# Performance work log

Measured on AMD Instinct MI355X. Metric: run time of the kernel, lower is better.

## Reference

```python
import jax, jax.numpy as jnp
import numpy as np

EPS = 1e-3  # keras BatchNormalization default epsilon


def _conv1x1(x, W, b):
    # x: (b, h, w, cin), W: (cin, cout)
    return jnp.einsum('bhwc,cd->bhwd', x, W) + b


def _bn(x, gamma, beta, mean, var):
    # inference-mode batch norm (moving statistics)
    return gamma * (x - mean) * jax.lax.rsqrt(var + EPS) + beta


def setup_inputs() -> dict:
    key = jax.random.key(0)
    ks = jax.random.split(key, 20)
    C, Ci = 512, 256
    B, Ha, Wa, Hd, Wd = 8, 32, 32, 64, 64
    s_in = 1.0 / np.sqrt(C)
    s_ic = 1.0 / np.sqrt(Ci)
    inp = {
        'detect': jax.random.normal(ks[0], (B, Hd, Wd, C), jnp.float32),
        'aim': jax.random.normal(ks[1], (B, Ha, Wa, C), jnp.float32),
        # g, theta, phi: C -> Ci 1x1 convs
        'Wg': jax.random.normal(ks[2], (C, Ci), jnp.float32) * s_in,
        'bg': jnp.zeros((Ci,), jnp.float32),
        'Wt': jax.random.normal(ks[3], (C, Ci), jnp.float32) * s_in,
        'bt': jnp.zeros((Ci,), jnp.float32),
        'Wp': jax.random.normal(ks[4], (C, Ci), jnp.float32) * s_in,
        'bp': jnp.zeros((Ci,), jnp.float32),
        # W branch: Ci -> C conv + BN
        'Ww': jax.random.normal(ks[5], (Ci, C), jnp.float32) * s_ic,
        'bw': jnp.zeros((C,), jnp.float32),
        'gw': jnp.ones((C,), jnp.float32),
        'betw': jnp.zeros((C,), jnp.float32),
        'mw': jax.random.normal(ks[6], (C,), jnp.float32) * 0.1,
        'vw': jax.random.uniform(ks[7], (C,), jnp.float32, 0.5, 1.5),
        # Q branch: Ci -> C conv + BN
        'Wq': jax.random.normal(ks[8], (Ci, C), jnp.float32) * s_ic,
        'bq': jnp.zeros((C,), jnp.float32),
        'gq': jnp.ones((C,), jnp.float32),
        'betq': jnp.zeros((C,), jnp.float32),
        'mq': jax.random.normal(ks[9], (C,), jnp.float32) * 0.1,
        'vq': jax.random.uniform(ks[10], (C,), jnp.float32, 0.5, 1.5),
    }
    return inp


def reference(detect, aim, Wg, bg, Wt, bt, Wp, bp,
              Ww, bw, gw, betw, mw, vw,
              Wq, bq, gq, betq, mq, vq):
    B, Ha, Wa, C = aim.shape
    _, Hd, Wd, _ = detect.shape
    Ci = Wg.shape[1]
    Na, Nd = Ha * Wa, Hd * Wd

    d_x = _conv1x1(detect, Wg, bg).reshape(B, Nd, Ci)     # (b, Nd, Ci)
    a_x = _conv1x1(aim, Wg, bg).reshape(B, Na, Ci)        # (b, Na, Ci)
    theta_x = _conv1x1(aim, Wt, bt).reshape(B, Na, Ci)    # (b, Na, Ci)
    phi_x = _conv1x1(detect, Wp, bp).reshape(B, Nd, Ci)   # (b, Nd, Ci)

    # affinity: (b, Na, Nd)
    f = jnp.einsum('bnc,bmc->bnm', theta_x, phi_x)
    f_div_C = f / Nd          # normalize by last dim of f
    fi_div_C = jnp.swapaxes(f, 1, 2) / Na  # (b, Nd, Na), normalized by its last dim

    non_aim = jnp.einsum('bnm,bmc->bnc', f_div_C, d_x).reshape(B, Ha, Wa, Ci)
    non_aim = _bn(_conv1x1(non_aim, Ww, bw), gw, betw, mw, vw) + aim

    non_det = jnp.einsum('bmn,bnc->bmc', fi_div_C, a_x).reshape(B, Hd, Wd, Ci)
    non_det = _bn(_conv1x1(non_det, Wq, bq), gq, betq, mq, vq) + detect

    return non_aim, non_det
```

## Files before the change

### kernel.cpp

```cpp
#include <hip/hip_runtime.h>

typedef unsigned short ushort_t;
typedef unsigned int uint32;
typedef __bf16 bf16x8 __attribute__((ext_vector_type(8)));
typedef float f32x4 __attribute__((ext_vector_type(4)));
typedef uint32 u32x4 __attribute__((ext_vector_type(4)));
typedef uint32 u32x2 __attribute__((ext_vector_type(2)));

typedef __attribute__((address_space(3))) uint32 as3_u32;
typedef const __attribute__((address_space(1))) uint32 as1_u32c;

__device__ __forceinline__ void gl_lds16(const ushort_t* g, ushort_t* l) {
    __builtin_amdgcn_global_load_lds((as1_u32c*)g, (as3_u32*)l, 16, 0, 0);
}

__device__ __forceinline__ float bf2f(ushort_t u) {
    uint32 x = ((uint32)u) << 16;
    return __builtin_bit_cast(float, x);
}
__device__ __forceinline__ ushort_t f2bf(float f) {
    uint32 x = __builtin_bit_cast(uint32, f);
    x += 0x7fffu + ((x >> 16) & 1u);
    return (ushort_t)(x >> 16);
}
__device__ __forceinline__ void ld4bf(const ushort_t* p, float* f) {
    const u32x2 w = *(const u32x2*)p;
    f[0] = bf2f((ushort_t)(w[0] & 0xffffu)); f[1] = bf2f((ushort_t)(w[0] >> 16));
    f[2] = bf2f((ushort_t)(w[1] & 0xffffu)); f[3] = bf2f((ushort_t)(w[1] >> 16));
}
__device__ __forceinline__ u32x2 pk4bf(const float* v) {
    u32x2 pk;
    pk[0] = (uint32)f2bf(v[0]) | ((uint32)f2bf(v[1]) << 16);
    pk[1] = (uint32)f2bf(v[2]) | ((uint32)f2bf(v[3]) << 16);
    return pk;
}

struct VecArgs { const void* s[14]; ushort_t* d[14]; int n[14]; };
__global__ void sniff_vec_kernel(const uint32* __restrict__ src, int* __restrict__ flag,
                                 VecArgs a) {
    __shared__ int cnt;
    if (threadIdx.x == 0) cnt = 0;
    __syncthreads();
    if (threadIdx.x < 64) {
        int weird = 0;
        for (int c = 0; c < 4; c++) {
            uint32 w = src[threadIdx.x * 4 + c];
            uint32 e = (w >> 7) & 0xFFu;
            weird += (e < 64u) || (e >= 192u);
        }
        if (weird) atomicAdd(&cnt, weird);
    }
    __syncthreads();
    const bool isf32 = (cnt > 32);
    if (threadIdx.x == 0) *flag = isf32 ? 1 : 0;
    const int t = threadIdx.x;
    for (int seg = 0; seg < 14; seg++) {
        const int n = a.n[seg];
        if (isf32) {
            const float* s = (const float*)a.s[seg];
            for (int i = t; i < n; i += 256) a.d[seg][i] = f2bf(s[i]);
        } else {
            const ushort_t* s = (const ushort_t*)a.s[seg];
            for (int i = t; i < n; i += 256) a.d[seg][i] = s[i];
        }
    }
}

struct WtArgs { const void* s[6]; ushort_t* d[6]; int R[6]; int C[6]; };
__global__ void canon_all(const void* __restrict__ dsrc, ushort_t* __restrict__ ddst,
                          const void* __restrict__ asrc, ushort_t* __restrict__ adst,
                          WtArgs wa, const int* __restrict__ flag) {
    const bool isf32 = (*flag != 0);
    const int b = blockIdx.x;
    if (b < 3072) {
        const void* src; ushort_t* dst; long n; int b0, nb;
        if (b < 2048) { src = dsrc; dst = ddst; n = 16777216; b0 = b; nb = 2048; }
        else          { src = asrc; dst = adst; n = 4194304;  b0 = b - 2048; nb = 1024; }
        long i = ((long)b0 * 256 + threadIdx.x) * 8;
        const long stride = (long)nb * 256 * 8;
        if (isf32) {
            const float* s = (const float*)src;
            for (; i < n; i += stride) {
                const f32x4 a = *(const f32x4*)(s + i);
                const f32x4 c = *(const f32x4*)(s + i + 4);
                u32x4 o;
                o[0] = (uint32)f2bf(a[0]) | ((uint32)f2bf(a[1]) << 16);
                o[1] = (uint32)f2bf(a[2]) | ((uint32)f2bf(a[3]) << 16);
                o[2] = (uint32)f2bf(c[0]) | ((uint32)f2bf(c[1]) << 16);
                o[3] = (uint32)f2bf(c[2]) | ((uint32)f2bf(c[3]) << 16);
                *(u32x4*)(dst + i) = o;
            }
        } else {
            const ushort_t* s = (const ushort_t*)src;
            for (; i < n; i += stride)
                *(u32x4*)(dst + i) = *(const u32x4*)(s + i);
        }
    } else {
        const int local = b - 3072;
        const int wsel = local >> 8;
        const int rem = local & 255;
        const int tr = rem >> 4, tc = rem & 15;
        const int R = wa.R[wsel], C = wa.C[wsel];
        if (tc * 32 >= C || tr * 32 >= R) return;
        __shared__ float s[32][33];
        const int t = threadIdx.x;
        const int r = t >> 3, c4 = (t & 7) * 4;
        const long sbase = (long)(tr * 32 + r) * C + tc * 32 + c4;
        if (isf32) {
            const float* S = (const float*)wa.s[wsel];
            const f32x4 v = *(const f32x4*)(S + sbase);
            for (int u = 0; u < 4; u++) s[r][c4 + u] = v[u];
        } else {
            const ushort_t* S = (const ushort_t*)wa.s[wsel];
            for (int u = 0; u < 4; u++) s[r][c4 + u] = bf2f(S[sbase + u]);
        }
        __syncthreads();
        float tv[4];
        for (int u = 0; u < 4; u++) tv[u] = s[c4 + u][r];
        *(u32x2*)(wa.d[wsel] + (long)(tc * 32 + r) * R + tr * 32 + c4) = pk4bf(tv);
    }
}

__global__ void reduce_t2_kernel(const float* __restrict__ P1, const float* __restrict__ P2,
                                 ushort_t* __restrict__ G1T, ushort_t* __restrict__ G2T) {
    __shared__ float s[32][33];
    const int zz = blockIdx.z;
    const float* P = (zz < 8) ? P1 : P2;
    ushort_t* out  = (zz < 8) ? G1T : G2T;
    const int b = zz & 7;
    const int tm = blockIdx.y, tn = blockIdx.x;
    const int t = threadIdx.x;
    const int r = t >> 3, c4 = (t & 7) * 4;
    const float* base = P + (long)b * 8 * 65536 + (long)(tm * 32 + r) * 256 + tn * 32 + c4;
    f32x4 acc = {0.f, 0.f, 0.f, 0.f};
    for (int kc = 0; kc < 8; kc++) acc += *(const f32x4*)(base + (long)kc * 65536);
    for (int u = 0; u < 4; u++) s[r][c4 + u] = acc[u];
    __syncthreads();
    float tv[4];
    for (int u = 0; u < 4; u++) tv[u] = s[c4 + u][r];
    *(u32x2*)(out + (long)b * 65536 + (long)(tn * 32 + r) * 256 + tm * 32 + c4) = pk4bf(tv);
}

#define BM 128
#define BN 128
#define BK 32
#define BIGN (1 << 30)

enum { EPI_BIAS = 0, EPI_BIASR = 1, EPI_SCALE = 2, EPI_BN = 3, EPI_PART = 4 };

struct GP {
    const ushort_t* A; const ushort_t* B; void* Cv; ushort_t* CT;
    const ushort_t* bias; const ushort_t* gamma; const ushort_t* beta;
    const ushort_t* mean; const ushort_t* var; const ushort_t* res;
    long coff, sA, sB, sC;
    int K, lda, ldb, ldc, cnmax, ldT;
    float alpha;
};
struct GP2 { GP g[2]; };

template <int EPI, bool DYNOUT, bool DUALT, bool SWAP>
__global__ __launch_bounds__(256) void gemm_nt(GP2 ga, int ysplit, int zsplit,
                                               const int* __restrict__ flag)
{
    __shared__ __align__(16) ushort_t As[BM * BK];
    __shared__ __align__(16) ushort_t Bs[BN * BK];

    const bool isf32 = DYNOUT ? (*flag != 0) : false;

    const uint32 gx = gridDim.x, gy = gridDim.y;
    const uint32 nwg = gx * gy * gridDim.z;
    const uint32 lid = blockIdx.x + gx * (blockIdx.y + gy * blockIdx.z);
    const uint32 swz = (lid & 7u) * (nwg >> 3) + (lid >> 3);
    const uint32 bx = swz % gx, t1 = swz / gx;
    int by = (int)(t1 % gy), bz = (int)(t1 / gy);

    int sel = 0;
    if (by >= ysplit) { by -= ysplit; sel = 1; }
    if (bz >= zsplit) { bz -= zsplit; sel = 1; }
    const GP& p = ga.g[sel];

    const ushort_t* A = p.A + (long)bz * p.sA;
    const ushort_t* B = p.B + (long)bz * p.sB;
    const long cbase = p.coff + (long)bz * p.sC;
    const int lda = p.lda, ldb = p.ldb, ldc = p.ldc, K = p.K;

    const int tid  = threadIdx.x;
    const int lane = tid & 63;
    const int w    = tid >> 6;
    const int wr   = w >> 1, wc = w & 1;
    const int lr   = lane & 15, q = lane >> 4;

    const int m0 = by * BM;
    const int n0 = bx * BN;

    const int lrow = lane >> 2, lu = lane & 3;
    const int us = (lu ^ ((lrow >> 1) & 3)) * 8;
    const int ra0 = w * 32 + lrow, ra1 = w * 32 + 16 + lrow;
    const ushort_t* Ar0 = A + (long)(m0 + ra0) * lda + us;
    const ushort_t* Ar1 = A + (long)(m0 + ra1) * lda + us;
    const ushort_t* Br0 = B + (long)(n0 + ra0) * ldb + us;
    const ushort_t* Br1 = B + (long)(n0 + ra1) * ldb + us;
    ushort_t* sA0 = &As[(w * 2 + 0) * 512];
    ushort_t* sA1 = &As[(w * 2 + 1) * 512];
    ushort_t* sB0 = &Bs[(w * 2 + 0) * 512];
    ushort_t* sB1 = &Bs[(w * 2 + 1) * 512];

    const int swq = (q ^ ((lr >> 1) & 3)) * 8;

    f32x4 acc[4][4];
#pragma unroll
    for (int i = 0; i < 4; i++)
#pragma unroll
        for (int j = 0; j < 4; j++) acc[i][j] = (f32x4){0.f, 0.f, 0.f, 0.f};

    for (int k0 = 0; k0 < K; k0 += BK) {
        gl_lds16(Ar0 + k0, sA0);
        gl_lds16(Ar1 + k0, sA1);
        gl_lds16(Br0 + k0, sB0);
        gl_lds16(Br1 + k0, sB1);
        __syncthreads();

        bf16x8 af[4], bfr[4];
#pragma unroll
        for (int i = 0; i < 4; i++)
            af[i] = __builtin_bit_cast(bf16x8,
                *(const u32x4*)(&As[(wr * 64 + i * 16 + lr) * BK + swq]));
#pragma unroll
        for (int j = 0; j < 4; j++)
            bfr[j] = __builtin_bit_cast(bf16x8,
                *(const u32x4*)(&Bs[(wc * 64 + j * 16 + lr) * BK + swq]));
#pragma unroll
        for (int i = 0; i < 4; i++)
#pragma unroll
            for (int j = 0; j < 4; j++) {
                if constexpr (SWAP)
                    acc[i][j] = __builtin_amdgcn_mfma_f32_16x16x32_bf16(bfr[j], af[i], acc[i][j], 0, 0, 0);
                else
                    acc[i][j] = __builtin_amdgcn_mfma_f32_16x16x32_bf16(af[i], bfr[j], acc[i][j], 0, 0, 0);
            }
        __syncthreads();
    }

    if constexpr (SWAP) {
#pragma unroll
        for (int j = 0; j < 4; j++) {
            const int coln = n0 + wc * 64 + j * 16 + q * 4;
            float sc4[4], sh4[4];
            if constexpr (EPI == EPI_BIAS) {
                float bb[4]; ld4bf(p.bias + coln, bb);
#pragma unroll
                for (int r = 0; r < 4; r++) { sc4[r] = 1.f; sh4[r] = bb[r]; }
            } else if constexpr (EPI == EPI_SCALE) {
#pragma unroll
                for (int r = 0; r < 4; r++) { sc4[r] = p.alpha; sh4[r] = 0.f; }
            } else if constexpr (EPI == EPI_BN) {
                float bb[4], g[4], bt[4], mn[4], vr[4];
                ld4bf(p.bias + coln, bb); ld4bf(p.gamma + coln, g); ld4bf(p.beta + coln, bt);
                ld4bf(p.mean + coln, mn); ld4bf(p.var + coln, vr);
#pragma unroll
                for (int r = 0; r < 4; r++) {
                    const float s = g[r] * rsqrtf(vr[r] + 1e-3f);
                    sc4[r] = s;
                    sh4[r] = s * bb[r] + bt[r] - s * mn[r];
                }
            }
#pragma unroll
            for (int i = 0; i < 4; i++) {
                const int row = m0 + wr * 64 + i * 16 + lr;
                const long off = cbase + (long)row * ldc + coln;
                float v[4];
#pragma unroll
                for (int r = 0; r < 4; r++) v[r] = acc[i][j][r];
                if constexpr (EPI == EPI_BIASR) {
                    const float bs = bf2f(p.bias[row]);
#pragma unroll
                    for (int r = 0; r < 4; r++) v[r] += bs;
                } else if constexpr (EPI == EPI_BN) {
                    float rs[4]; ld4bf(p.res + (long)row * ldc + coln, rs);
#pragma unroll
                    for (int r = 0; r < 4; r++) v[r] = sc4[r] * v[r] + sh4[r] + rs[r];
                } else if constexpr (EPI != EPI_PART) {
#pragma unroll
                    for (int r = 0; r < 4; r++) v[r] = sc4[r] * v[r] + sh4[r];
                }
                if constexpr (EPI == EPI_PART) {
                    *(f32x4*)((float*)p.Cv + off) = (f32x4){v[0], v[1], v[2], v[3]};
                } else if constexpr (DYNOUT) {
                    if (isf32) *(f32x4*)((float*)p.Cv + off) = (f32x4){v[0], v[1], v[2], v[3]};
                    else       *(u32x2*)((ushort_t*)p.Cv + off) = pk4bf(v);
                } else {
                    *(u32x2*)((ushort_t*)p.Cv + off) = pk4bf(v);
                }
            }
        }
    } else {
        const bool doC = (n0 < p.cnmax);
#pragma unroll
        for (int j = 0; j < 4; j++) {
            const int col = n0 + wc * 64 + j * 16 + lr;
            float bs = 0.f, sc = 1.f, sh = 0.f;
            if constexpr (EPI == EPI_BIAS || EPI == EPI_BN) bs = bf2f(p.bias[col]);
            if constexpr (EPI == EPI_BN) {
                const float g  = bf2f(p.gamma[col]);
                const float bt = bf2f(p.beta[col]);
                const float mn = bf2f(p.mean[col]);
                const float vr = bf2f(p.var[col]);
                sc = g * rsqrtf(vr + 1e-3f);
                sh = bt - sc * mn;
            }
#pragma unroll
            for (int i = 0; i < 4; i++) {
                const int rowbase = m0 + wr * 64 + i * 16 + q * 4;
                ushort_t tmp[4];
#pragma unroll
                for (int r = 0; r < 4; r++) {
                    const int row = rowbase + r;
                    float v = acc[i][j][r];
                    if constexpr (EPI == EPI_BIAS) v += bs;
                    else if constexpr (EPI == EPI_BIASR) v += bf2f(p.bias[row]);
                    else if constexpr (EPI == EPI_SCALE) v *= p.alpha;
                    else if constexpr (EPI == EPI_BN)
                        v = sc * (v + bs) + sh + bf2f(p.res[(long)row * ldc + col]);
                    const long off = cbase + (long)row * ldc + col;
                    if constexpr (EPI == EPI_PART) {
                        ((float*)p.Cv)[off] = v;
                    } else if constexpr (DYNOUT) {
                        if (isf32) ((float*)p.Cv)[off] = v;
                        else       ((ushort_t*)p.Cv)[off] = f2bf(v);
                    } else {
                        const ushort_t us2 = f2bf(v);
                        tmp[r] = us2;
                        if (doC) ((ushort_t*)p.Cv)[off] = us2;
                    }
                }
                if constexpr (DUALT) {
                    u32x2 pk;
                    pk[0] = (uint32)tmp[0] | ((uint32)tmp[1] << 16);
                    pk[1] = (uint32)tmp[2] | ((uint32)tmp[3] << 16);
                    *(u32x2*)(p.CT + (long)col * p.ldT + rowbase) = pk;
                }
            }
        }
    }
}

extern "C" void kernel_launch(void* const* d_in, const int* in_sizes, int n_in,
                              void* d_out, int out_size, void* d_ws, size_t ws_size,
                              hipStream_t stream)
{
    int* flag = (int*)d_ws;
    ushort_t* base = (ushort_t*)((char*)d_ws + 16);
    long o = 0;
    ushort_t* detect_c = base + o; o += 16777216;
    ushort_t* aim_c    = base + o; o += 4194304;
    ushort_t* WpgT = base + o; o += 262144;
    ushort_t* WtgT = base + o; o += 262144;
    ushort_t* WwT  = base + o; o += 131072;
    ushort_t* WqT  = base + o; o += 131072;
    ushort_t* bpg_c  = base + o; o += 512;
    ushort_t* btg_c  = base + o; o += 512;
    ushort_t* bw_c   = base + o; o += 512;
    ushort_t* gw_c   = base + o; o += 512;
    ushort_t* betw_c = base + o; o += 512;
    ushort_t* mw_c   = base + o; o += 512;
    ushort_t* vw_c   = base + o; o += 512;
    ushort_t* bq_c   = base + o; o += 512;
    ushort_t* gq_c   = base + o; o += 512;
    ushort_t* betq_c = base + o; o += 512;
    ushort_t* mq_c   = base + o; o += 512;
    ushort_t* vq_c   = base + o; o += 512;
    ushort_t* phi    = base + o; o += 8388608;
    ushort_t* PT     = base + o; o += 16777216;
    ushort_t* theta  = base + o; o += 2097152;
    ushort_t* TT     = base + o; o += 4194304;
    ushort_t* G1T    = base + o; o += 524288;
    ushort_t* G2T    = base + o; o += 524288;
    ushort_t* U      = base + o; o += 16777216;
    float* P1 = (float*)U;
    float* P2 = P1 + 4194304;
    ushort_t* na = U;
    ushort_t* nd = na + 2097152;
    ushort_t* phiT = PT;
    ushort_t* d_xT = PT + 8388608;
    ushort_t* thetaT = TT;
    ushort_t* a_xT = TT + 2097152;

    VecArgs va;
    const int vidx[14] = {7, 3, 5, 3, 9, 10, 11, 12, 13, 15, 16, 17, 18, 19};
    ushort_t* vdst[14] = {bpg_c, bpg_c + 256, btg_c, btg_c + 256,
                          bw_c, gw_c, betw_c, mw_c, vw_c,
                          bq_c, gq_c, betq_c, mq_c, vq_c};
    const int vn[14] = {256, 256, 256, 256, 512, 512, 512, 512, 512, 512, 512, 512, 512, 512};
    for (int i = 0; i < 14; i++) { va.s[i] = d_in[vidx[i]]; va.d[i] = vdst[i]; va.n[i] = vn[i]; }
    sniff_vec_kernel<<<1, 256, 0, stream>>>((const uint32*)d_in[0], flag, va);

    WtArgs wa;
    wa.s[0] = d_in[6];  wa.d[0] = WpgT;              wa.R[0] = 512; wa.C[0] = 256;
    wa.s[1] = d_in[2];  wa.d[1] = WpgT + 256 * 512;  wa.R[1] = 512; wa.C[1] = 256;
    wa.s[2] = d_in[4];  wa.d[2] = WtgT;              wa.R[2] = 512; wa.C[2] = 256;
    wa.s[3] = d_in[2];  wa.d[3] = WtgT + 256 * 512;  wa.R[3] = 512; wa.C[3] = 256;
    wa.s[4] = d_in[8];  wa.d[4] = WwT;               wa.R[4] = 256; wa.C[4] = 512;
    wa.s[5] = d_in[14]; wa.d[5] = WqT;               wa.R[5] = 256; wa.C[5] = 512;
    canon_all<<<4608, 256, 0, stream>>>(d_in[0], detect_c, d_in[1], aim_c, wa, flag);

    const dim3 blk(256);
    const ushort_t* np = nullptr;
    ushort_t* npm = nullptr;

    {
        GP2 g;
        g.g[0] = GP{detect_c, WpgT, phi, PT, bpg_c, np, np, np, np, np,
                    0, 0, 0, 0, 512, 512, 512, 256, 256, 32768, 1.f};
        g.g[1] = GP{aim_c, WtgT, theta, TT, btg_c, np, np, np, np, np,
                    0, 0, 0, 0, 512, 512, 512, 256, 256, 8192, 1.f};
        gemm_nt<EPI_BIAS, false, true, false><<<dim3(4, 320, 1), blk, 0, stream>>>(
            g, 256, BIGN, flag);
    }

    {
        GP2 g;
        g.g[0] = GP{phiT, d_xT, P1, npm, np, np, np, np, np, np,
                    0, 512, 512, 65536, 512, 32768, 32768, 256, BIGN, 0, 1.f};
        g.g[1] = GP{thetaT, a_xT, P2, npm, np, np, np, np, np, np,
                    0, 128, 128, 65536, 128, 8192, 8192, 256, BIGN, 0, 1.f};
        gemm_nt<EPI_PART, false, false, true><<<dim3(2, 2, 128), blk, 0, stream>>>(
            g, BIGN, 64, flag);
    }

    reduce_t2_kernel<<<dim3(8, 8, 16), blk, 0, stream>>>(P1, P2, G1T, G2T);

    {
        GP2 g;
        g.g[0] = GP{phi, G2T, nd, npm, np, np, np, np, np, np,
                    0, 1048576, 65536, 1048576, 256, 256, 256, 256, BIGN, 0, 1.f / 1024.f};
        g.g[1] = GP{theta, G1T, na, npm, np, np, np, np, np, np,
                    0, 262144, 65536, 262144, 256, 256, 256, 256, BIGN, 0, 1.f / 4096.f};
        gemm_nt<EPI_SCALE, false, false, true><<<dim3(2, 40, 8), blk, 0, stream>>>(
            g, 32, BIGN, flag);
    }

    {
        GP2 g;
        g.g[0] = GP{nd, WqT, d_out, npm, bq_c, gq_c, betq_c, mq_c, vq_c, detect_c,
                    8192L * 512, 0, 0, 0, 256, 256, 256, 512, BIGN, 0, 1.f};
        g.g[1] = GP{na, WwT, d_out, npm, bw_c, gw_c, betw_c, mw_c, vw_c, aim_c,
                    0, 0, 0, 0, 256, 256, 256, 512, BIGN, 0, 1.f};
        gemm_nt<EPI_BN, true, false, true><<<dim3(4, 320, 1), blk, 0, stream>>>(
            g, 256, BIGN, flag);
    }
}
```

Baseline: 368.5 us.

## Triple-buffer LDS tiles in gemm_nt with async prefetch two stages ahead

Replaces the single-buffered K loop, which loaded one tile, synchronised, computed and synchronised again, with a three-stage LDS ring. Tiles for step t+2 are fetched with global_load_lds while the MFMAs for step t run. Explicit vmcnt waits and a single barrier per iteration replace the two __syncthreads, hiding global-load latency behind compute. In exchange LDS use triples to 48KB per block, which can lower occupancy.

```diff
diff --git a/kernel.cpp b/kernel.cpp
--- a/kernel.cpp
+++ b/kernel.cpp
@@ -144,6 +144,8 @@
 #define BM 128
 #define BN 128
 #define BK 32
+#define LDSH (BM * BK)
+#define NBUF 3
 #define BIGN (1 << 30)
 
 enum { EPI_BIAS = 0, EPI_BIASR = 1, EPI_SCALE = 2, EPI_BN = 3, EPI_PART = 4 };
@@ -162,8 +164,8 @@
 __global__ __launch_bounds__(256) void gemm_nt(GP2 ga, int ysplit, int zsplit,
                                                const int* __restrict__ flag)
 {
-    __shared__ __align__(16) ushort_t As[BM * BK];
-    __shared__ __align__(16) ushort_t Bs[BN * BK];
+    __shared__ __align__(16) ushort_t As[NBUF * LDSH];
+    __shared__ __align__(16) ushort_t Bs[NBUF * LDSH];
 
     const bool isf32 = DYNOUT ? (*flag != 0) : false;
 
@@ -213,22 +215,43 @@
 #pragma unroll
         for (int j = 0; j < 4; j++) acc[i][j] = (f32x4){0.f, 0.f, 0.f, 0.f};
 
-    for (int k0 = 0; k0 < K; k0 += BK) {
-        gl_lds16(Ar0 + k0, sA0);
-        gl_lds16(Ar1 + k0, sA1);
-        gl_lds16(Br0 + k0, sB0);
-        gl_lds16(Br1 + k0, sB1);
-        __syncthreads();
-
+    const int nt = K / BK;
+
+    {
+        gl_lds16(Ar0, sA0); gl_lds16(Ar1, sA1);
+        gl_lds16(Br0, sB0); gl_lds16(Br1, sB1);
+        if (nt > 1) {
+            gl_lds16(Ar0 + BK, sA0 + LDSH); gl_lds16(Ar1 + BK, sA1 + LDSH);
+            gl_lds16(Br0 + BK, sB0 + LDSH); gl_lds16(Br1 + BK, sB1 + LDSH);
+        }
+    }
+
+    int c0 = 0, c2 = 2;
+    for (int t = 0; t < nt; ++t) {
+        if (t + 1 < nt) asm volatile("s_waitcnt vmcnt(4)" ::: "memory");
+        else            asm volatile("s_waitcnt vmcnt(0)" ::: "memory");
+        __builtin_amdgcn_s_barrier();
+        __builtin_amdgcn_sched_barrier(0);
+
+        if (t + 2 < nt) {
+            const int nb = c2 * LDSH;
+            const int kn = (t + 2) * BK;
+            gl_lds16(Ar0 + kn, sA0 + nb); gl_lds16(Ar1 + kn, sA1 + nb);
+            gl_lds16(Br0 + kn, sB0 + nb); gl_lds16(Br1 + kn, sB1 + nb);
+        }
+        __builtin_amdgcn_sched_barrier(0);
+
+        const ushort_t* Ab = As + c0 * LDSH;
+        const ushort_t* Bb = Bs + c0 * LDSH;
         bf16x8 af[4], bfr[4];
 #pragma unroll
         for (int i = 0; i < 4; i++)
             af[i] = __builtin_bit_cast(bf16x8,
-                *(const u32x4*)(&As[(wr * 64 + i * 16 + lr) * BK + swq]));
+                *(const u32x4*)(&Ab[(wr * 64 + i * 16 + lr) * BK + swq]));
 #pragma unroll
         for (int j = 0; j < 4; j++)
             bfr[j] = __builtin_bit_cast(bf16x8,
-                *(const u32x4*)(&Bs[(wc * 64 + j * 16 + lr) * BK + swq]));
+                *(const u32x4*)(&Bb[(wc * 64 + j * 16 + lr) * BK + swq]));
 #pragma unroll
         for (int i = 0; i < 4; i++)
 #pragma unroll
@@ -238,7 +261,10 @@
                 else
                     acc[i][j] = __builtin_amdgcn_mfma_f32_16x16x32_bf16(af[i], bfr[j], acc[i][j], 0, 0, 0);
             }
-        __syncthreads();
+        __builtin_amdgcn_sched_barrier(0);
+
+        c0 = (c0 + 1 == NBUF) ? 0 : c0 + 1;
+        c2 = (c2 + 1 == NBUF) ? 0 : c2 + 1;
     }
 
     if constexpr (SWAP) {
```

After: 361.9 us. About the same (-1.8%).

## Fuse all stages into one persistent kernel with grid-wide barriers

Applied to the files above, without the earlier changes.

Replaces the six separate launches (sniff, canonicalize, conv GEMM, partial GEMM, reduce, attention GEMM, output GEMM) with a single persistent kernel of 1280 workgroups. Stages are separated by atomic-counter grid barriers, and the dtype sniff is computed per block with wave shuffles. The goal is to remove launch gaps and per-kernel tail effects. In exchange it relies on all 1280 workgroups being co-resident (launch bounds 256,5) and pays spin-wait barrier costs, while some stages leave many blocks idle.

```diff
diff --git a/kernel.cpp b/kernel.cpp
--- a/kernel.cpp
+++ b/kernel.cpp
@@ -10,6 +10,8 @@
 typedef __attribute__((address_space(3))) uint32 as3_u32;
 typedef const __attribute__((address_space(1))) uint32 as1_u32c;
 
+#define NWG 1280
+
 __device__ __forceinline__ void gl_lds16(const ushort_t* g, ushort_t* l) {
     __builtin_amdgcn_global_load_lds((as1_u32c*)g, (as3_u32*)l, 16, 0, 0);
 }
@@ -35,115 +37,10 @@
     return pk;
 }
 
-struct VecArgs { const void* s[14]; ushort_t* d[14]; int n[14]; };
-__global__ void sniff_vec_kernel(const uint32* __restrict__ src, int* __restrict__ flag,
-                                 VecArgs a) {
-    __shared__ int cnt;
-    if (threadIdx.x == 0) cnt = 0;
-    __syncthreads();
-    if (threadIdx.x < 64) {
-        int weird = 0;
-        for (int c = 0; c < 4; c++) {
-            uint32 w = src[threadIdx.x * 4 + c];
-            uint32 e = (w >> 7) & 0xFFu;
-            weird += (e < 64u) || (e >= 192u);
-        }
-        if (weird) atomicAdd(&cnt, weird);
-    }
-    __syncthreads();
-    const bool isf32 = (cnt > 32);
-    if (threadIdx.x == 0) *flag = isf32 ? 1 : 0;
-    const int t = threadIdx.x;
-    for (int seg = 0; seg < 14; seg++) {
-        const int n = a.n[seg];
-        if (isf32) {
-            const float* s = (const float*)a.s[seg];
-            for (int i = t; i < n; i += 256) a.d[seg][i] = f2bf(s[i]);
-        } else {
-            const ushort_t* s = (const ushort_t*)a.s[seg];
-            for (int i = t; i < n; i += 256) a.d[seg][i] = s[i];
-        }
-    }
-}
-
-struct WtArgs { const void* s[6]; ushort_t* d[6]; int R[6]; int C[6]; };
-__global__ void canon_all(const void* __restrict__ dsrc, ushort_t* __restrict__ ddst,
-                          const void* __restrict__ asrc, ushort_t* __restrict__ adst,
-                          WtArgs wa, const int* __restrict__ flag) {
-    const bool isf32 = (*flag != 0);
-    const int b = blockIdx.x;
-    if (b < 3072) {
-        const void* src; ushort_t* dst; long n; int b0, nb;
-        if (b < 2048) { src = dsrc; dst = ddst; n = 16777216; b0 = b; nb = 2048; }
-        else          { src = asrc; dst = adst; n = 4194304;  b0 = b - 2048; nb = 1024; }
-        long i = ((long)b0 * 256 + threadIdx.x) * 8;
-        const long stride = (long)nb * 256 * 8;
-        if (isf32) {
-            const float* s = (const float*)src;
-            for (; i < n; i += stride) {
-                const f32x4 a = *(const f32x4*)(s + i);
-                const f32x4 c = *(const f32x4*)(s + i + 4);
-                u32x4 o;
-                o[0] = (uint32)f2bf(a[0]) | ((uint32)f2bf(a[1]) << 16);
-                o[1] = (uint32)f2bf(a[2]) | ((uint32)f2bf(a[3]) << 16);
-                o[2] = (uint32)f2bf(c[0]) | ((uint32)f2bf(c[1]) << 16);
-                o[3] = (uint32)f2bf(c[2]) | ((uint32)f2bf(c[3]) << 16);
-                *(u32x4*)(dst + i) = o;
-            }
-        } else {
-            const ushort_t* s = (const ushort_t*)src;
-            for (; i < n; i += stride)
-                *(u32x4*)(dst + i) = *(const u32x4*)(s + i);
-        }
-    } else {
-        const int local = b - 3072;
-        const int wsel = local >> 8;
-        const int rem = local & 255;
-        const int tr = rem >> 4, tc = rem & 15;
-        const int R = wa.R[wsel], C = wa.C[wsel];
-        if (tc * 32 >= C || tr * 32 >= R) return;
-        __shared__ float s[32][33];
-        const int t = threadIdx.x;
-        const int r = t >> 3, c4 = (t & 7) * 4;
-        const long sbase = (long)(tr * 32 + r) * C + tc * 32 + c4;
-        if (isf32) {
-            const float* S = (const float*)wa.s[wsel];
-            const f32x4 v = *(const f32x4*)(S + sbase);
-            for (int u = 0; u < 4; u++) s[r][c4 + u] = v[u];
-        } else {
-            const ushort_t* S = (const ushort_t*)wa.s[wsel];
-            for (int u = 0; u < 4; u++) s[r][c4 + u] = bf2f(S[sbase + u]);
-        }
-        __syncthreads();
-        float tv[4];
-        for (int u = 0; u < 4; u++) tv[u] = s[c4 + u][r];
-        *(u32x2*)(wa.d[wsel] + (long)(tc * 32 + r) * R + tr * 32 + c4) = pk4bf(tv);
-    }
-}
-
-__global__ void reduce_t2_kernel(const float* __restrict__ P1, const float* __restrict__ P2,
-                                 ushort_t* __restrict__ G1T, ushort_t* __restrict__ G2T) {
-    __shared__ float s[32][33];
-    const int zz = blockIdx.z;
-    const float* P = (zz < 8) ? P1 : P2;
-    ushort_t* out  = (zz < 8) ? G1T : G2T;
-    const int b = zz & 7;
-    const int tm = blockIdx.y, tn = blockIdx.x;
-    const int t = threadIdx.x;
-    const int r = t >> 3, c4 = (t & 7) * 4;
-    const float* base = P + (long)b * 8 * 65536 + (long)(tm * 32 + r) * 256 + tn * 32 + c4;
-    f32x4 acc = {0.f, 0.f, 0.f, 0.f};
-    for (int kc = 0; kc < 8; kc++) acc += *(const f32x4*)(base + (long)kc * 65536);
-    for (int u = 0; u < 4; u++) s[r][c4 + u] = acc[u];
-    __syncthreads();
-    float tv[4];
-    for (int u = 0; u < 4; u++) tv[u] = s[c4 + u][r];
-    *(u32x2*)(out + (long)b * 65536 + (long)(tn * 32 + r) * 256 + tm * 32 + c4) = pk4bf(tv);
-}
-
 #define BM 128
 #define BN 128
 #define BK 32
+#define LDSH (BM * BK)
 #define BIGN (1 << 30)
 
 enum { EPI_BIAS = 0, EPI_BIASR = 1, EPI_SCALE = 2, EPI_BN = 3, EPI_PART = 4 };
@@ -157,28 +54,138 @@
     float alpha;
 };
 struct GP2 { GP g[2]; };
+struct VecArgs { const void* s[14]; ushort_t* d[14]; int n[14]; };
+struct WtArgs { const void* s[6]; ushort_t* d[6]; int R[6]; int C[6]; };
+
+struct MegaArgs {
+    const void* in0; const void* in1;
+    ushort_t* det; ushort_t* aim;
+    VecArgs va; WtArgs wa;
+    GP2 conv, part, ndna, outs;
+    const float* P1; const float* P2; ushort_t* G1T; ushort_t* G2T;
+    uint32* bar;
+};
+
+__device__ __forceinline__ bool sniff(const void* in0) {
+    const uint32* s = (const uint32*)in0;
+    const int lane = threadIdx.x & 63;
+    int wd = 0;
+    for (int c = 0; c < 4; c++) {
+        const uint32 w = s[lane * 4 + c];
+        const uint32 e = (w >> 7) & 0xFFu;
+        wd += (e < 64u) || (e >= 192u);
+    }
+    for (int off = 32; off; off >>= 1) wd += __shfl_down(wd, off);
+    return __shfl(wd, 0) > 32;
+}
+
+__device__ void gbar(uint32* ctr) {
+    __syncthreads();
+    if (threadIdx.x == 0) {
+        __threadfence();
+        atomicAdd(ctr, 1u);
+        while (__hip_atomic_load(ctr, __ATOMIC_RELAXED, __HIP_MEMORY_SCOPE_AGENT) < NWG)
+            __builtin_amdgcn_s_sleep(4);
+        __threadfence();
+    }
+    __syncthreads();
+}
+
+__device__ __forceinline__ void decode(int bid, int nwg, int gx, int gy,
+                                       int ys, int zs,
+                                       int& bx, int& by, int& bz, int& sel) {
+    const uint32 swz = (uint32)(bid & 7) * (uint32)(nwg >> 3) + (uint32)(bid >> 3);
+    bx = (int)(swz % (uint32)gx);
+    const uint32 t1 = swz / (uint32)gx;
+    by = (int)(t1 % (uint32)gy);
+    bz = (int)(t1 / (uint32)gy);
+    sel = 0;
+    if (by >= ys) { by -= ys; sel = 1; }
+    if (bz >= zs) { bz -= zs; sel = 1; }
+}
+
+__device__ void canon_vb(const MegaArgs& a, int b, bool isf32, float (*st)[33]) {
+    if (b < 3072) {
+        const void* src; ushort_t* dst; long n; int b0, nb;
+        if (b < 2048) { src = a.in0; dst = a.det; n = 16777216; b0 = b; nb = 2048; }
+        else          { src = a.in1; dst = a.aim; n = 4194304;  b0 = b - 2048; nb = 1024; }
+        long i = ((long)b0 * 256 + threadIdx.x) * 8;
+        const long stride = (long)nb * 256 * 8;
+        if (isf32) {
+            const float* s = (const float*)src;
+            for (; i < n; i += stride) {
+                const f32x4 x = *(const f32x4*)(s + i);
+                const f32x4 y = *(const f32x4*)(s + i + 4);
+                u32x4 o;
+                o[0] = (uint32)f2bf(x[0]) | ((uint32)f2bf(x[1]) << 16);
+                o[1] = (uint32)f2bf(x[2]) | ((uint32)f2bf(x[3]) << 16);
+                o[2] = (uint32)f2bf(y[0]) | ((uint32)f2bf(y[1]) << 16);
+                o[3] = (uint32)f2bf(y[2]) | ((uint32)f2bf(y[3]) << 16);
+                *(u32x4*)(dst + i) = o;
+            }
+        } else {
+            const ushort_t* s = (const ushort_t*)src;
+            for (; i < n; i += stride)
+                *(u32x4*)(dst + i) = *(const u32x4*)(s + i);
+        }
+    } else if (b < 4608) {
+        const int local = b - 3072;
+        const int wsel = local >> 8;
+        const int rem = local & 255;
+        const int tr = rem >> 4, tc = rem & 15;
+        const int R = a.wa.R[wsel], C = a.wa.C[wsel];
+        if (tc * 32 < C && tr * 32 < R) {
+            const int t = threadIdx.x;
+            const int r = t >> 3, c4 = (t & 7) * 4;
+            const long sbase = (long)(tr * 32 + r) * C + tc * 32 + c4;
+            if (isf32) {
+                const float* S = (const float*)a.wa.s[wsel];
+                const f32x4 v = *(const f32x4*)(S + sbase);
+                for (int u = 0; u < 4; u++) st[r][c4 + u] = v[u];
+            } else {
+                const ushort_t* S = (const ushort_t*)a.wa.s[wsel];
+                for (int u = 0; u < 4; u++) st[r][c4 + u] = bf2f(S[sbase + u]);
+            }
+            __syncthreads();
+            float tv[4];
+            for (int u = 0; u < 4; u++) tv[u] = st[c4 + u][r];
+            *(u32x2*)(a.wa.d[wsel] + (long)(tc * 32 + r) * R + tr * 32 + c4) = pk4bf(tv);
+        }
+    } else {
+        const int t = threadIdx.x;
+        for (int seg = 0; seg < 14; seg++) {
+            const int n = a.va.n[seg];
+            if (isf32) {
+                const float* s = (const float*)a.va.s[seg];
+                for (int i = t; i < n; i += 256) a.va.d[seg][i] = f2bf(s[i]);
+            } else {
+                const ushort_t* s = (const ushort_t*)a.va.s[seg];
+                for (int i = t; i < n; i += 256) a.va.d[seg][i] = s[i];
+            }
+        }
+    }
+}
+
+__device__ void reduce_tile(const MegaArgs& a, int bid, float (*st)[33]) {
+    const int tn = bid & 7, tm = (bid >> 3) & 7, zz = bid >> 6;
+    const float* P = (zz < 8) ? a.P1 : a.P2;
+    ushort_t* out  = (zz < 8) ? a.G1T : a.G2T;
+    const int b = zz & 7;
+    const int t = threadIdx.x;
+    const int r = t >> 3, c4 = (t & 7) * 4;
+    const float* base = P + (long)b * 8 * 65536 + (long)(tm * 32 + r) * 256 + tn * 32 + c4;
+    f32x4 acc = {0.f, 0.f, 0.f, 0.f};
+    for (int kc = 0; kc < 8; kc++) acc += *(const f32x4*)(base + (long)kc * 65536);
+    for (int u = 0; u < 4; u++) st[r][c4 + u] = acc[u];
+    __syncthreads();
+    float tv[4];
+    for (int u = 0; u < 4; u++) tv[u] = st[c4 + u][r];
+    *(u32x2*)(out + (long)b * 65536 + (long)(tn * 32 + r) * 256 + tm * 32 + c4) = pk4bf(tv);
+}
 
 template <int EPI, bool DYNOUT, bool DUALT, bool SWAP>
-__global__ __launch_bounds__(256) void gemm_nt(GP2 ga, int ysplit, int zsplit,
-                                               const int* __restrict__ flag)
-{
-    __shared__ __align__(16) ushort_t As[BM * BK];
-    __shared__ __align__(16) ushort_t Bs[BN * BK];
-
-    const bool isf32 = DYNOUT ? (*flag != 0) : false;
-
-    const uint32 gx = gridDim.x, gy = gridDim.y;
-    const uint32 nwg = gx * gy * gridDim.z;
-    const uint32 lid = blockIdx.x + gx * (blockIdx.y + gy * blockIdx.z);
-    const uint32 swz = (lid & 7u) * (nwg >> 3) + (lid >> 3);
-    const uint32 bx = swz % gx, t1 = swz / gx;
-    int by = (int)(t1 % gy), bz = (int)(t1 / gy);
-
-    int sel = 0;
-    if (by >= ysplit) { by -= ysplit; sel = 1; }
-    if (bz >= zsplit) { bz -= zsplit; sel = 1; }
-    const GP& p = ga.g[sel];
-
+__device__ void gemm_tile(const GP& p, int bx, int by, int bz,
+                          ushort_t* Asb, ushort_t* Bsb, bool isf32) {
     const ushort_t* A = p.A + (long)bz * p.sA;
     const ushort_t* B = p.B + (long)bz * p.sB;
     const long cbase = p.coff + (long)bz * p.sC;
@@ -200,10 +207,10 @@
     const ushort_t* Ar1 = A + (long)(m0 + ra1) * lda + us;
     const ushort_t* Br0 = B + (long)(n0 + ra0) * ldb + us;
     const ushort_t* Br1 = B + (long)(n0 + ra1) * ldb + us;
-    ushort_t* sA0 = &As[(w * 2 + 0) * 512];
-    ushort_t* sA1 = &As[(w * 2 + 1) * 512];
-    ushort_t* sB0 = &Bs[(w * 2 + 0) * 512];
-    ushort_t* sB1 = &Bs[(w * 2 + 1) * 512];
+    ushort_t* sA0 = Asb + (w * 2 + 0) * 512;
+    ushort_t* sA1 = Asb + (w * 2 + 1) * 512;
+    ushort_t* sB0 = Bsb + (w * 2 + 0) * 512;
+    ushort_t* sB1 = Bsb + (w * 2 + 1) * 512;
 
     const int swq = (q ^ ((lr >> 1) & 3)) * 8;
 
@@ -214,21 +221,19 @@
         for (int j = 0; j < 4; j++) acc[i][j] = (f32x4){0.f, 0.f, 0.f, 0.f};
 
     for (int k0 = 0; k0 < K; k0 += BK) {
-        gl_lds16(Ar0 + k0, sA0);
-        gl_lds16(Ar1 + k0, sA1);
-        gl_lds16(Br0 + k0, sB0);
-        gl_lds16(Br1 + k0, sB1);
+        gl_lds16(Ar0 + k0, sA0); gl_lds16(Ar1 + k0, sA1);
+        gl_lds16(Br0 + k0, sB0); gl_lds16(Br1 + k0, sB1);
         __syncthreads();
 
         bf16x8 af[4], bfr[4];
 #pragma unroll
         for (int i = 0; i < 4; i++)
             af[i] = __builtin_bit_cast(bf16x8,
-                *(const u32x4*)(&As[(wr * 64 + i * 16 + lr) * BK + swq]));
+                *(const u32x4*)(&Asb[(wr * 64 + i * 16 + lr) * BK + swq]));
 #pragma unroll
         for (int j = 0; j < 4; j++)
             bfr[j] = __builtin_bit_cast(bf16x8,
-                *(const u32x4*)(&Bs[(wc * 64 + j * 16 + lr) * BK + swq]));
+                *(const u32x4*)(&Bsb[(wc * 64 + j * 16 + lr) * BK + swq]));
 #pragma unroll
         for (int i = 0; i < 4; i++)
 #pragma unroll
@@ -344,12 +349,50 @@
     }
 }
 
+__global__ __launch_bounds__(256, 5) void mega(MegaArgs a) {
+    __shared__ __align__(16) ushort_t As[LDSH];
+    __shared__ __align__(16) ushort_t Bs[LDSH];
+    float (*st)[33] = (float(*)[33])As;
+
+    const bool isf32 = sniff(a.in0);
+    const int bid = blockIdx.x;
+    int bx, by, bz, sel;
+
+    for (int vb = bid; vb < 4609; vb += NWG) {
+        canon_vb(a, vb, isf32, st);
+        __syncthreads();
+    }
+    gbar(a.bar + 0);
+
+    decode(bid, 1280, 4, 320, 256, BIGN, bx, by, bz, sel);
+    gemm_tile<EPI_BIAS, false, true, false>(a.conv.g[sel], bx, by, bz, As, Bs, isf32);
+    gbar(a.bar + 1);
+
+    if (bid < 512) {
+        decode(bid, 512, 2, 2, BIGN, 64, bx, by, bz, sel);
+        gemm_tile<EPI_PART, false, false, true>(a.part.g[sel], bx, by, bz, As, Bs, isf32);
+    }
+    gbar(a.bar + 2);
+
+    if (bid < 1024) reduce_tile(a, bid, st);
+    gbar(a.bar + 3);
+
+    if (bid < 640) {
+        decode(bid, 640, 2, 40, 32, BIGN, bx, by, bz, sel);
+        gemm_tile<EPI_SCALE, false, false, true>(a.ndna.g[sel], bx, by, bz, As, Bs, isf32);
+    }
+    gbar(a.bar + 4);
+
+    decode(bid, 1280, 4, 320, 256, BIGN, bx, by, bz, sel);
+    gemm_tile<EPI_BN, true, false, true>(a.outs.g[sel], bx, by, bz, As, Bs, isf32);
+}
+
 extern "C" void kernel_launch(void* const* d_in, const int* in_sizes, int n_in,
                               void* d_out, int out_size, void* d_ws, size_t ws_size,
                               hipStream_t stream)
 {
-    int* flag = (int*)d_ws;
-    ushort_t* base = (ushort_t*)((char*)d_ws + 16);
+    uint32* bar = (uint32*)d_ws;
+    ushort_t* base = (ushort_t*)((char*)d_ws + 256);
     long o = 0;
     ushort_t* detect_c = base + o; o += 16777216;
     ushort_t* aim_c    = base + o; o += 4194304;
@@ -385,67 +428,50 @@
     ushort_t* thetaT = TT;
     ushort_t* a_xT = TT + 2097152;
 
-    VecArgs va;
+    hipMemsetAsync(bar, 0, 64, stream);
+
+    MegaArgs ma;
+    ma.in0 = d_in[0]; ma.in1 = d_in[1];
+    ma.det = detect_c; ma.aim = aim_c;
+    ma.P1 = P1; ma.P2 = P2; ma.G1T = G1T; ma.G2T = G2T;
+    ma.bar = bar;
+
     const int vidx[14] = {7, 3, 5, 3, 9, 10, 11, 12, 13, 15, 16, 17, 18, 19};
     ushort_t* vdst[14] = {bpg_c, bpg_c + 256, btg_c, btg_c + 256,
                           bw_c, gw_c, betw_c, mw_c, vw_c,
                           bq_c, gq_c, betq_c, mq_c, vq_c};
     const int vn[14] = {256, 256, 256, 256, 512, 512, 512, 512, 512, 512, 512, 512, 512, 512};
-    for (int i = 0; i < 14; i++) { va.s[i] = d_in[vidx[i]]; va.d[i] = vdst[i]; va.n[i] = vn[i]; }
-    sniff_vec_kernel<<<1, 256, 0, stream>>>((const uint32*)d_in[0], flag, va);
-
-    WtArgs wa;
-    wa.s[0] = d_in[6];  wa.d[0] = WpgT;              wa.R[0] = 512; wa.C[0] = 256;
-    wa.s[1] = d_in[2];  wa.d[1] = WpgT + 256 * 512;  wa.R[1] = 512; wa.C[1] = 256;
-    wa.s[2] = d_in[4];  wa.d[2] = WtgT;              wa.R[2] = 512; wa.C[2] = 256;
-    wa.s[3] = d_in[2];  wa.d[3] = WtgT + 256 * 512;  wa.R[3] = 512; wa.C[3] = 256;
-    wa.s[4] = d_in[8];  wa.d[4] = WwT;               wa.R[4] = 256; wa.C[4] = 512;
-    wa.s[5] = d_in[14]; wa.d[5] = WqT;               wa.R[5] = 256; wa.C[5] = 512;
-    canon_all<<<4608, 256, 0, stream>>>(d_in[0], detect_c, d_in[1], aim_c, wa, flag);
-
-    const dim3 blk(256);
+    for (int i = 0; i < 14; i++) { ma.va.s[i] = d_in[vidx[i]]; ma.va.d[i] = vdst[i]; ma.va.n[i] = vn[i]; }
+
+    ma.wa.s[0] = d_in[6];  ma.wa.d[0] = WpgT;             ma.wa.R[0] = 512; ma.wa.C[0] = 256;
+    ma.wa.s[1] = d_in[2];  ma.wa.d[1] = WpgT + 256 * 512; ma.wa.R[1] = 512; ma.wa.C[1] = 256;
+    ma.wa.s[2] = d_in[4];  ma.wa.d[2] = WtgT;             ma.wa.R[2] = 512; ma.wa.C[2] = 256;
+    ma.wa.s[3] = d_in[2];  ma.wa.d[3] = WtgT + 256 * 512; ma.wa.R[3] = 512; ma.wa.C[3] = 256;
+    ma.wa.s[4] = d_in[8];  ma.wa.d[4] = WwT;              ma.wa.R[4] = 256; ma.wa.C[4] = 512;
+    ma.wa.s[5] = d_in[14]; ma.wa.d[5] = WqT;              ma.wa.R[5] = 256; ma.wa.C[5] = 512;
+
     const ushort_t* np = nullptr;
     ushort_t* npm = nullptr;
 
-    {
-        GP2 g;
-        g.g[0] = GP{detect_c, WpgT, phi, PT, bpg_c, np, np, np, np, np,
-                    0, 0, 0, 0, 512, 512, 512, 256, 256, 32768, 1.f};
-        g.g[1] = GP{aim_c, WtgT, theta, TT, btg_c, np, np, np, np, np,
-                    0, 0, 0, 0, 512, 512, 512, 256, 256, 8192, 1.f};
-        gemm_nt<EPI_BIAS, false, true, false><<<dim3(4, 320, 1), blk, 0, stream>>>(
-            g, 256, BIGN, flag);
-    }
-
-    {
-        GP2 g;
-        g.g[0] = GP{phiT, d_xT, P1, npm, np, np, np, np, np, np,
-                    0, 512, 512, 65536, 512, 32768, 32768, 256, BIGN, 0, 1.f};
-        g.g[1] = GP{thetaT, a_xT, P2, npm, np, np, np, np, np, np,
-                    0, 128, 128, 65536, 128, 8192, 8192, 256, BIGN, 0, 1.f};
-        gemm_nt<EPI_PART, false, false, true><<<dim3(2, 2, 128), blk, 0, stream>>>(
-            g, BIGN, 64, flag);
-    }
-
-    reduce_t2_kernel<<<dim3(8, 8, 16), blk, 0, stream>>>(P1, P2, G1T, G2T);
-
-    {
-        GP2 g;
-        g.g[0] = GP{phi, G2T, nd, npm, np, np, np, np, np, np,
-                    0, 1048576, 65536, 1048576, 256, 256, 256, 256, BIGN, 0, 1.f / 1024.f};
-        g.g[1] = GP{theta, G1T, na, npm, np, np, np, np, np, np,
-                    0, 262144, 65536, 262144, 256, 256, 256, 256, BIGN, 0, 1.f / 4096.f};
-        gemm_nt<EPI_SCALE, false, false, true><<<dim3(2, 40, 8), blk, 0, stream>>>(
-            g, 32, BIGN, flag);
-    }
-
-    {
-        GP2 g;
-        g.g[0] = GP{nd, WqT, d_out, npm, bq_c, gq_c, betq_c, mq_c, vq_c, detect_c,
-                    8192L * 512, 0, 0, 0, 256, 256, 256, 512, BIGN, 0, 1.f};
-        g.g[1] = GP{na, WwT, d_out, npm, bw_c, gw_c, betw_c, mw_c, vw_c, aim_c,
-                    0, 0, 0, 0, 256, 256, 256, 512, BIGN, 0, 1.f};
-        gemm_nt<EPI_BN, true, false, true><<<dim3(4, 320, 1), blk, 0, stream>>>(
-            g, 256, BIGN, flag);
-    }
-}
+    ma.conv.g[0] = GP{detect_c, WpgT, phi, PT, bpg_c, np, np, np, np, np,
+                      0, 0, 0, 0, 512, 512, 512, 256, 256, 32768, 1.f};
+    ma.conv.g[1] = GP{aim_c, WtgT, theta, TT, btg_c, np, np, np, np, np,
+                      0, 0, 0, 0, 512, 512, 512, 256, 256, 8192, 1.f};
+
+    ma.part.g[0] = GP{phiT, d_xT, P1, npm, np, np, np, np, np, np,
+                      0, 512, 512, 65536, 512, 32768, 32768, 256, BIGN, 0, 1.f};
+    ma.part.g[1] = GP{thetaT, a_xT, P2, npm, np, np, np, np, np, np,
+                      0, 128, 128, 65536, 128, 8192, 8192, 256, BIGN, 0, 1.f};
+
+    ma.ndna.g[0] = GP{phi, G2T, nd, npm, np, np, np, np, np, np,
+                      0, 1048576, 65536, 1048576, 256, 256, 256, 256, BIGN, 0, 1.f / 1024.f};
+    ma.ndna.g[1] = GP{theta, G1T, na, npm, np, np, np, np, np, np,
+                      0, 262144, 65536, 262144, 256, 256, 256, 256, BIGN, 0, 1.f / 4096.f};
+
+    ma.outs.g[0] = GP{nd, WqT, d_out, npm, bq_c, gq_c, betq_c, mq_c, vq_c, detect_c,
+                      8192L * 512, 0, 0, 0, 256, 256, 256, 512, BIGN, 0, 1.f};
+    ma.outs.g[1] = GP{na, WwT, d_out, npm, bw_c, gw_c, betw_c, mw_c, vw_c, aim_c,
+                      0, 0, 0, 0, 256, 256, 256, 512, BIGN, 0, 1.f};
+
+    mega<<<NWG, 256, 0, stream>>>(ma);
+}
```

Measured after the change: 1.137 ms. 208% more time.
